# Performance work log

Hardware: AMD Instinct MI355X
Metric: run time of the kernel (lower is better)

The kernel has to match this reference:

```python
import jax, jax.numpy as jnp
import numpy as np
import math
from jax import lax

B, L = 64, 8192
S = L // 8          # width after 3 stride-(1,2) SAME convs
D = 4 * 5           # height(4) * channels(5) -> per-token feature dim
D_FLAT = S * D


def setup_inputs():
    key = jax.random.key(0)
    ks = jax.random.split(key, 32)
    sc = 0.1
    inp = {
        "inputs": jax.random.randint(ks[0], (B, L), 0, 4, dtype=jnp.int32),
        # conv stack: HWIO kernels, Conv2D(5,(4,4),(1,2),'SAME')
        "conv_w1": sc * jax.random.normal(ks[1], (4, 4, 1, 5), jnp.float32),
        "conv_b1": jnp.zeros((5,), jnp.float32),
        "conv_w2": sc * jax.random.normal(ks[2], (4, 4, 5, 5), jnp.float32),
        "conv_b2": jnp.zeros((5,), jnp.float32),
        "conv_w3": sc * jax.random.normal(ks[3], (4, 4, 5, 5), jnp.float32),
        "conv_b3": jnp.zeros((5,), jnp.float32),
        # 3 SelfAttn blocks, each with K/Q/V projections [D, D]
        "attn1_K": sc * jax.random.normal(ks[4], (D, D), jnp.float32),
        "attn1_Q": sc * jax.random.normal(ks[5], (D, D), jnp.float32),
        "attn1_V": sc * jax.random.normal(ks[6], (D, D), jnp.float32),
        "attn2_K": sc * jax.random.normal(ks[7], (D, D), jnp.float32),
        "attn2_Q": sc * jax.random.normal(ks[8], (D, D), jnp.float32),
        "attn2_V": sc * jax.random.normal(ks[9], (D, D), jnp.float32),
        "attn3_K": sc * jax.random.normal(ks[10], (D, D), jnp.float32),
        "attn3_Q": sc * jax.random.normal(ks[11], (D, D), jnp.float32),
        "attn3_V": sc * jax.random.normal(ks[12], (D, D), jnp.float32),
        # 3 Dense(10) layers (no activation, as in Keras defaults)
        "dense_w1": 0.01 * jax.random.normal(ks[13], (D_FLAT, 10), jnp.float32),
        "dense_b1": jnp.zeros((10,), jnp.float32),
        "dense_w2": sc * jax.random.normal(ks[14], (10, 10), jnp.float32),
        "dense_b2": jnp.zeros((10,), jnp.float32),
        "dense_w3": sc * jax.random.normal(ks[15], (10, 10), jnp.float32),
        "dense_b3": jnp.zeros((10,), jnp.float32),
    }
    return inp


def _conv(x, w, b):
    # NHWC, HWIO, strides (1,2), SAME
    y = lax.conv_general_dilated(x, w, window_strides=(1, 2), padding="SAME",
                                 dimension_numbers=("NHWC", "HWIO", "NHWC"))
    return y + b


def _self_attn(x, Kw, Qw, Vw):
    # x: [B, S, D]; manual causal scaled dot-product attention
    K = x @ Kw
    Q = x @ Qw
    V = x @ Vw
    s = Q.shape[1]
    mask = jnp.triu(jnp.full((s, s), -jnp.inf, dtype=x.dtype), k=1)
    scores = jnp.einsum("bsd,btd->bst", Q, K) / math.sqrt(K.shape[-1]) + mask
    return jax.nn.softmax(scores, axis=-1) @ V


def reference(inputs, conv_w1, conv_b1, conv_w2, conv_b2, conv_w3, conv_b3,
              attn1_K, attn1_Q, attn1_V, attn2_K, attn2_Q, attn2_V,
              attn3_K, attn3_Q, attn3_V,
              dense_w1, dense_b1, dense_w2, dense_b2, dense_w3, dense_b3):
    # one_hot over axis=1 -> [B, 4, L], then channel dim -> [B, 4, L, 1]
    x = jax.nn.one_hot(inputs, 4, axis=1, dtype=jnp.float32)[..., None]
    x = _conv(x, conv_w1, conv_b1)
    x = _conv(x, conv_w2, conv_b2)
    x = _conv(x, conv_w3, conv_b3)            # [B, 4, S, 5]
    # tokens along width, features = height(4) x channels(5)
    x = jnp.transpose(x, (0, 2, 1, 3)).reshape(x.shape[0], S, D)
    x = _self_attn(x, attn1_K, attn1_Q, attn1_V)
    x = _self_attn(x, attn2_K, attn2_Q, attn2_V)
    x = _self_attn(x, attn3_K, attn3_Q, attn3_V)
    x = x.reshape(x.shape[0], -1)             # flatten [B, S*D]
    x = x @ dense_w1 + dense_b1
    x = x @ dense_w2 + dense_b2
    x = x @ dense_w3 + dense_b3               # [B, 10]
    return x
```

## Files before the change

### kernel.cpp

```cpp
#include <hip/hip_runtime.h>
#include <hip/hip_bf16.h>


#define B_ 64
#define L_ 8192
#define S_ 1024
#define D_ 20

typedef unsigned short ushort_t;
typedef __attribute__((ext_vector_type(8))) short short8_t;
typedef __attribute__((ext_vector_type(4))) short short4_t;
typedef __attribute__((ext_vector_type(4))) float f32x4_t;

__device__ __forceinline__ ushort_t f2bf(float f) {
  unsigned u = __float_as_uint(f);
  return (ushort_t)((u + 0x7fffu + ((u >> 16) & 1u)) >> 16);
}
__device__ __forceinline__ float bf2f(ushort_t h) {
  return __uint_as_float(((unsigned)h) << 16);
}

__global__ __launch_bounds__(256) void conv12_kernel(
    const int* __restrict__ inp,
    const float* __restrict__ W1c, const float* __restrict__ B1c,
    const float* __restrict__ W2c, const float* __restrict__ B2c,
    float* __restrict__ out,
    const float* __restrict__ W1d,
    float* __restrict__ W1T,
    const float* __restrict__ B1d, const float* __restrict__ W2d,
    const float* __restrict__ B2d, const float* __restrict__ W3d,
    const float* __restrict__ B3d,
    float* __restrict__ outp) {
  __shared__ float w1s[80], b1s[5], w2s[400], b2s[5];
  for (int j = threadIdx.x; j < 400; j += 256) w2s[j] = W2c[j];
  if (threadIdx.x < 80)      w1s[threadIdx.x]      = W1c[threadIdx.x];
  else if (threadIdx.x < 85) b1s[threadIdx.x - 80] = B1c[threadIdx.x - 80];
  else if (threadIdx.x < 90) b2s[threadIdx.x - 85] = B2c[threadIdx.x - 85];
  __syncthreads();
  const int idx = blockIdx.x * 256 + threadIdx.x;
  const int b  = idx >> 11;
  const int wo = idx & 2047;
  const int* ib = inp + (size_t)b * L_;
  int iv[10];
#pragma unroll
  for (int t = 0; t < 10; ++t) {
    int g = 4 * wo - 3 + t;
    iv[t] = (g >= 0 && g < L_) ? ib[g] : -100;
  }
  float val[4][4][5];
#pragma unroll
  for (int pos = 0; pos < 4; ++pos) {
    const int w1 = 2 * wo - 1 + pos;
    const bool okp = (w1 >= 0 && w1 < 4096);
#pragma unroll
    for (int hi = 0; hi < 4; ++hi)
#pragma unroll
      for (int ci = 0; ci < 5; ++ci) val[hi][pos][ci] = okp ? b1s[ci] : 0.f;
    if (okp) {
#pragma unroll
      for (int kw = 0; kw < 4; ++kw) {
        const int gw = 2 * w1 - 1 + kw;
        if (gw >= 0 && gw < L_) {
          const int v = iv[2 * pos + kw];
#pragma unroll
          for (int hi = 0; hi < 4; ++hi) {
            const int kh = v - hi + 1;
            if (kh >= 0 && kh < 4) {
#pragma unroll
              for (int ci = 0; ci < 5; ++ci)
                val[hi][pos][ci] += w1s[(kh * 4 + kw) * 5 + ci];
            }
          }
        }
      }
    }
  }
  float acc[4][5];
#pragma unroll
  for (int h = 0; h < 4; ++h)
#pragma unroll
    for (int c = 0; c < 5; ++c) acc[h][c] = b2s[c];
#pragma unroll
  for (int kh = 0; kh < 4; ++kh)
#pragma unroll
    for (int kw = 0; kw < 4; ++kw)
#pragma unroll
      for (int ci = 0; ci < 5; ++ci) {
        const float* wp = w2s + ((kh * 4 + kw) * 5 + ci) * 5;
        float w0 = wp[0], w1v = wp[1], w2v = wp[2], w3 = wp[3], w4 = wp[4];
#pragma unroll
        for (int h = 0; h < 4; ++h) {
          int hi = h - 1 + kh;
          if (hi >= 0 && hi < 4) {
            float x = val[hi][kw][ci];
            acc[h][0] += w0 * x;  acc[h][1] += w1v * x; acc[h][2] += w2v * x;
            acc[h][3] += w3 * x;  acc[h][4] += w4 * x;
          }
        }
      }
  float* ob = out + (size_t)b * 4 * 2048 * 5;
#pragma unroll
  for (int h = 0; h < 4; ++h)
#pragma unroll
    for (int c = 0; c < 5; ++c) ob[(h * 2048 + wo) * 5 + c] = acc[h][c];
  for (int j = idx; j < 204800; j += 131072) {
    const int col = j / 20480, i2 = j - col * 20480;
    float w23[10];
#pragma unroll
    for (int k2 = 0; k2 < 10; ++k2) {
      float s = 0.f;
#pragma unroll
      for (int m = 0; m < 10; ++m) s += W2d[k2 * 10 + m] * W3d[m * 10 + col];
      w23[k2] = s;
    }
    float s = 0.f;
#pragma unroll
    for (int k2 = 0; k2 < 10; ++k2) s += W1d[i2 * 10 + k2] * w23[k2];
    W1T[j] = s;
  }
  if (idx < 640) {
    const int col = idx - (idx / 10) * 10;
    float bc = B3d[col];
#pragma unroll
    for (int m = 0; m < 10; ++m) bc += B2d[m] * W3d[m * 10 + col];
#pragma unroll
    for (int k2 = 0; k2 < 10; ++k2) {
      float w23 = 0.f;
#pragma unroll
      for (int m = 0; m < 10; ++m) w23 += W2d[k2 * 10 + m] * W3d[m * 10 + col];
      bc += B1d[k2] * w23;
    }
    outp[idx] = bc;
  }
}

__global__ __launch_bounds__(256) void conv3_proj_kernel(
    const float* __restrict__ in,
    const float* __restrict__ W,  const float* __restrict__ Bi,
    const float* __restrict__ Kw, const float* __restrict__ Qw,
    const float* __restrict__ Vw,
    ushort_t* __restrict__ Qb, ushort_t* __restrict__ Kb,
    ushort_t* __restrict__ Vt) {
  constexpr int WIN = 2048;
  __shared__ float ws[400], bs[5];
  __shared__ float kw[400], qw[400], vw[400];
  for (int j = threadIdx.x; j < 400; j += 256) {
    ws[j] = W[j]; kw[j] = Kw[j]; qw[j] = Qw[j]; vw[j] = Vw[j];
  }
  if (threadIdx.x < 5) bs[threadIdx.x] = Bi[threadIdx.x];
  __syncthreads();
  const int r  = blockIdx.x * 256 + threadIdx.x;
  const int b  = r >> 10;
  const int wo = r & 1023;
  float val[4][4][5];
#pragma unroll
  for (int hi = 0; hi < 4; ++hi) {
    const float* ir = in + ((size_t)b * 4 + hi) * WIN * 5;
#pragma unroll
    for (int kwp = 0; kwp < 4; ++kwp) {
      int wi = 2 * wo - 1 + kwp;
      bool ok = (wi >= 0 && wi < WIN);
#pragma unroll
      for (int ci = 0; ci < 5; ++ci) val[hi][kwp][ci] = ok ? ir[wi * 5 + ci] : 0.f;
    }
  }
  float acc[4][5];
#pragma unroll
  for (int h = 0; h < 4; ++h)
#pragma unroll
    for (int c = 0; c < 5; ++c) acc[h][c] = bs[c];
#pragma unroll
  for (int kh = 0; kh < 4; ++kh)
#pragma unroll
    for (int kwp = 0; kwp < 4; ++kwp)
#pragma unroll
      for (int ci = 0; ci < 5; ++ci) {
        const float* wp = ws + ((kh * 4 + kwp) * 5 + ci) * 5;
        float w0 = wp[0], w1 = wp[1], w2 = wp[2], w3 = wp[3], w4 = wp[4];
#pragma unroll
        for (int h = 0; h < 4; ++h) {
          int hi = h - 1 + kh;
          if (hi >= 0 && hi < 4) {
            float x = val[hi][kwp][ci];
            acc[h][0] += w0 * x; acc[h][1] += w1 * x; acc[h][2] += w2 * x;
            acc[h][3] += w3 * x; acc[h][4] += w4 * x;
          }
        }
      }
  float x[D_];
#pragma unroll
  for (int h = 0; h < 4; ++h)
#pragma unroll
    for (int c = 0; c < 5; ++c) x[h * 5 + c] = acc[h][c];
  float q[D_], k[D_], v[D_];
#pragma unroll
  for (int j = 0; j < D_; ++j) { q[j] = 0.f; k[j] = 0.f; v[j] = 0.f; }
#pragma unroll
  for (int i = 0; i < D_; ++i) {
#pragma unroll
    for (int j = 0; j < D_; ++j) {
      q[j] += x[i] * qw[i * D_ + j];
      k[j] += x[i] * kw[i * D_ + j];
      v[j] += x[i] * vw[i * D_ + j];
    }
  }
  const float sc = 0.22360679774997896f;
  ushort_t qt[32], kt[32];
#pragma unroll
  for (int j = 0; j < D_; ++j) { qt[j] = f2bf(q[j] * sc); kt[j] = f2bf(k[j]); }
#pragma unroll
  for (int j = D_; j < 32; ++j) { qt[j] = 0; kt[j] = 0; }
  int4* qd = (int4*)(Qb + (size_t)r * 32);
  int4* kd = (int4*)(Kb + (size_t)r * 32);
#pragma unroll
  for (int j = 0; j < 4; ++j) {
    qd[j] = *(const int4*)(qt + 8 * j);
    kd[j] = *(const int4*)(kt + 8 * j);
  }
  ushort_t* vbase = Vt + ((size_t)b * 32) * 1024 + wo;
#pragma unroll
  for (int d = 0; d < D_; ++d) vbase[d * 1024] = f2bf(v[d]);
}

template <bool FUSE>
__global__ __launch_bounds__(512, 6) void attn_kernel(
    const ushort_t* __restrict__ Qb, const ushort_t* __restrict__ Kb,
    const ushort_t* __restrict__ Vt,
    const float* __restrict__ Kw2, const float* __restrict__ Qw2,
    const float* __restrict__ Vw2,
    ushort_t* __restrict__ Qb2, ushort_t* __restrict__ Kb2,
    ushort_t* __restrict__ Vt2,
    const float* __restrict__ W1T,
    float* __restrict__ outp) {
  constexpr int VST = 1032;
  __shared__ ushort_t vts[20 * VST];
  __shared__ float extraf[FUSE ? 2480 : 1280];
  __shared__ float mrgL[64];
  __shared__ float red2[FUSE ? 4 : 40];
  const int blk   = blockIdx.x;
  const int b     = blk & 63;
  const int strip = 15 - (blk >> 6);
  const int q0    = strip * 64;
  const int nt    = q0 + 64;
  const int tid   = threadIdx.x;
  const int w     = tid >> 6;
  const int sub   = w & 3;
  const int half  = w >> 2;
  const int lane  = tid & 63;
  const int n     = lane & 15;
  const int quad  = lane >> 4;
  const int qbase = q0 + 16 * sub;
  const int qg    = qbase + n;
  const ushort_t* VtB = Vt + (size_t)b * 32 * 1024;
  const int ntc = nt >> 3;
  for (int i = tid; i < 20 * ntc; i += 512) {
    int row = i / ntc, cc = i - row * ntc;
    *(int4*)(vts + row * VST + cc * 8) =
        *(const int4*)(VtB + (size_t)row * 1024 + cc * 8);
  }
  if (FUSE) {
    for (int j = tid; j < 1200; j += 512) {
      int m = j / 400, oo = j - m * 400;
      extraf[j] = (m == 0) ? Kw2[oo] : (m == 1) ? Qw2[oo] : Vw2[oo];
    }
  }
  const ushort_t* KbB = Kb + (size_t)b * 1024 * 32;
  short8_t qfrag = *(const short8_t*)(Qb + ((size_t)(b * 1024 + qbase + n)) * 32 + quad * 8);
  f32x4_t oA = {0.f, 0.f, 0.f, 0.f};
  f32x4_t oB = {0.f, 0.f, 0.f, 0.f};
  const f32x4_t zero = {0.f, 0.f, 0.f, 0.f};
  float lsum = 0.f;
  const int nt2 = nt >> 1;
  const int tlo = half ? nt2 : 0;
  int thi = half ? nt : nt2;
  if (thi > qbase + 16) thi = qbase + 16;
  __syncthreads();
  for (int t0 = tlo; t0 < thi; t0 += 32) {
    short8_t kf0 = *(const short8_t*)(KbB + (size_t)(t0 + n) * 32 + quad * 8);
    short8_t kf1 = *(const short8_t*)(KbB + (size_t)(t0 + 16 + n) * 32 + quad * 8);
#pragma unroll
    for (int c = 0; c < 2; ++c) {
      const int tg = t0 + c * 16 + quad * 4;
      f32x4_t s = __builtin_amdgcn_mfma_f32_16x16x32_bf16(c ? kf1 : kf0, qfrag,
                                                          zero, 0, 0, 0);
      ushort_t pk4[4];
#pragma unroll
      for (int r = 0; r < 4; ++r) {
        float p = (tg + r <= qg) ? __expf(s[r]) : 0.f;
        ushort_t h = f2bf(p);
        lsum += bf2f(h);
        pk4[r] = h;
      }
      short4_t pfrag = *(const short4_t*)pk4;
      short4_t vlo = *(const short4_t*)(vts + n * VST + t0 + c * 16 + quad * 4);
      short4_t vhi = *(const short4_t*)(vts + (16 + (n & 3)) * VST + t0 + c * 16 + quad * 4);
      oA = __builtin_amdgcn_mfma_f32_16x16x16bf16_1k(vlo, pfrag, oA, 0, 0, 0);
      oB = __builtin_amdgcn_mfma_f32_16x16x16bf16_1k(vhi, pfrag, oB, 0, 0, 0);
    }
  }
  float l = lsum;
  l += __shfl_xor(l, 16, 64);
  l += __shfl_xor(l, 32, 64);
  float* ox  = FUSE ? (extraf + 1200) : extraf;
  float* oxw = ox + sub * 320;
  if (half) {
#pragma unroll
    for (int r = 0; r < 4; ++r) oxw[n * 20 + quad * 4 + r] = oA[r];
    if (quad == 0) {
#pragma unroll
      for (int r = 0; r < 4; ++r) oxw[n * 20 + 16 + r] = oB[r];
      mrgL[sub * 16 + n] = l;
    }
  }
  __syncthreads();
  if (!half) {
#pragma unroll
    for (int r = 0; r < 4; ++r) oA[r] += oxw[n * 20 + quad * 4 + r];
    if (quad == 0) {
#pragma unroll
      for (int r = 0; r < 4; ++r) oB[r] += oxw[n * 20 + 16 + r];
    }
    l += mrgL[sub * 16 + n];
    const float inv = 1.f / l;
#pragma unroll
    for (int r = 0; r < 4; ++r) oxw[n * 20 + quad * 4 + r] = oA[r] * inv;
    if (quad == 0) {
#pragma unroll
      for (int r = 0; r < 4; ++r) oxw[n * 20 + 16 + r] = oB[r] * inv;
    }
  }
  if (FUSE) {
    if (!half) {
      float* pw = extraf;
      __asm__ volatile("s_waitcnt lgkmcnt(0)" ::: "memory");
      const int row  = lane >> 2;
      const int part = lane & 3;
      float x[D_];
#pragma unroll
      for (int i = 0; i < D_; ++i) x[i] = oxw[row * 20 + i];
      float qv[5], kv[5], vv[5];
#pragma unroll
      for (int jj = 0; jj < 5; ++jj) { qv[jj] = 0.f; kv[jj] = 0.f; vv[jj] = 0.f; }
#pragma unroll
      for (int i = 0; i < D_; ++i) {
        const float xi = x[i];
#pragma unroll
        for (int jj = 0; jj < 5; ++jj) {
          const int j = 5 * part + jj;
          kv[jj] += xi * pw[i * 20 + j];
          qv[jj] += xi * pw[400 + i * 20 + j];
          vv[jj] += xi * pw[800 + i * 20 + j];
        }
      }
      const float sc = 0.22360679774997896f;
      const int rg = b * 1024 + qbase + row;
      const int s  = rg & 1023;
#pragma unroll
      for (int jj = 0; jj < 5; ++jj) {
        const int j = 5 * part + jj;
        Kb2[(size_t)rg * 32 + j] = f2bf(kv[jj]);
        Qb2[(size_t)rg * 32 + j] = f2bf(qv[jj] * sc);
        Vt2[(size_t)b * 32768 + (size_t)j * 1024 + s] = f2bf(vv[jj]);
      }
      if (part == 0) {
#pragma unroll
        for (int u = 0; u < 6; ++u)
          *(unsigned*)(Kb2 + (size_t)rg * 32 + 20 + 2 * u) = 0u;
      } else if (part == 1) {
#pragma unroll
        for (int u = 0; u < 6; ++u)
          *(unsigned*)(Qb2 + (size_t)rg * 32 + 20 + 2 * u) = 0u;
      }
    }
  } else {
    __syncthreads();
    float acc[10];
#pragma unroll
    for (int j = 0; j < 10; ++j) acc[j] = 0.f;
    const int base = q0 * 20;
    if (tid < 256) {
#pragma unroll
      for (int k = 0; k < 5; ++k) {
        const int il = tid + 256 * k;
        const float xv = ox[il];
#pragma unroll
        for (int j = 0; j < 10; ++j)
          acc[j] += xv * W1T[(size_t)j * 20480 + base + il];
      }
    }
#pragma unroll
    for (int off = 1; off < 64; off <<= 1) {
#pragma unroll
      for (int j = 0; j < 10; ++j) acc[j] += __shfl_xor(acc[j], off, 64);
    }
    if (tid < 256 && lane == 0) {
#pragma unroll
      for (int j = 0; j < 10; ++j) red2[w * 10 + j] = acc[j];
    }
    __syncthreads();
    if (tid < 10) {
      float s2 = red2[tid] + red2[10 + tid] + red2[20 + tid] + red2[30 + tid];
      atomicAdd(&outp[b * 10 + tid], s2);
    }
  }
}

extern "C" void kernel_launch(void* const* d_in, const int* in_sizes, int n_in,
                              void* d_out, int out_size, void* d_ws, size_t ws_size,
                              hipStream_t stream) {
  const int*   inp = (const int*)d_in[0];
  const float* cw1 = (const float*)d_in[1];
  const float* cb1 = (const float*)d_in[2];
  const float* cw2 = (const float*)d_in[3];
  const float* cb2 = (const float*)d_in[4];
  const float* cw3 = (const float*)d_in[5];
  const float* cb3 = (const float*)d_in[6];
  const float* a1K = (const float*)d_in[7];
  const float* a1Q = (const float*)d_in[8];
  const float* a1V = (const float*)d_in[9];
  const float* a2K = (const float*)d_in[10];
  const float* a2Q = (const float*)d_in[11];
  const float* a2V = (const float*)d_in[12];
  const float* a3K = (const float*)d_in[13];
  const float* a3Q = (const float*)d_in[14];
  const float* a3V = (const float*)d_in[15];
  const float* dw1 = (const float*)d_in[16];
  const float* db1 = (const float*)d_in[17];
  const float* dw2 = (const float*)d_in[18];
  const float* db2 = (const float*)d_in[19];
  const float* dw3 = (const float*)d_in[20];
  const float* db3 = (const float*)d_in[21];
  float* outp = (float*)d_out;

  float* wsf = (float*)d_ws;
  ushort_t* qbA  = (ushort_t*)(wsf);
  ushort_t* kbA  = (ushort_t*)(wsf + 1048576);
  ushort_t* vtA  = (ushort_t*)(wsf + 2097152);
  float*    w1t  = wsf + 4466688;
  ushort_t* qbB  = (ushort_t*)(wsf + 4671488);
  ushort_t* kbB  = (ushort_t*)(wsf + 5712384);
  ushort_t* vtB  = (ushort_t*)(wsf + 6760960);
  float*    c2   = wsf + 5242880;

  conv12_kernel<<<512, 256, 0, stream>>>(inp, cw1, cb1, cw2, cb2, c2, dw1,
                                         w1t, db1, dw2, db2, dw3, db3, outp);

  conv3_proj_kernel<<<256, 256, 0, stream>>>(c2, cw3, cb3, a1K, a1Q, a1V,
                                             qbA, kbA, vtA);
  attn_kernel<true><<<1024, 512, 0, stream>>>(
      qbA, kbA, vtA, a2K, a2Q, a2V, qbB, kbB, vtB, nullptr, nullptr);
  attn_kernel<true><<<1024, 512, 0, stream>>>(
      qbB, kbB, vtB, a3K, a3Q, a3V, qbA, kbA, vtA, nullptr, nullptr);
  attn_kernel<false><<<1024, 512, 0, stream>>>(
      qbA, kbA, vtA, nullptr, nullptr, nullptr, nullptr, nullptr, nullptr,
      w1t, outp);
}
```

Measured before the change: 196.9 us.

## Fuse conv1-2 and conv3+QKV projection into one kernel via shared-memory tile

Merges the conv1/conv2 kernel and the conv3+projection kernel into a single launch. Each 512-thread block computes 514 conv2 output columns (a 256-wide tile plus halo) into shared memory, then half the threads run conv3 and the Q/K/V projection from that tile. This removes one kernel launch and the global round-trip of the conv2 intermediate, at the cost of recomputing two halo columns per tile, leaving half the threads idle in the second phase, and using fewer blocks.

```diff
diff --git a/kernel.cpp b/kernel.cpp
--- a/kernel.cpp
+++ b/kernel.cpp
@@ -20,11 +20,15 @@
   return __uint_as_float(((unsigned)h) << 16);
 }
 
-__global__ __launch_bounds__(256) void conv12_kernel(
+__global__ __launch_bounds__(512) void conv_fused_kernel(
     const int* __restrict__ inp,
     const float* __restrict__ W1c, const float* __restrict__ B1c,
     const float* __restrict__ W2c, const float* __restrict__ B2c,
-    float* __restrict__ out,
+    const float* __restrict__ W3c, const float* __restrict__ B3c,
+    const float* __restrict__ Kw,  const float* __restrict__ Qw,
+    const float* __restrict__ Vw,
+    ushort_t* __restrict__ Qb, ushort_t* __restrict__ Kb,
+    ushort_t* __restrict__ Vt,
     const float* __restrict__ W1d,
     float* __restrict__ W1T,
     const float* __restrict__ B1d, const float* __restrict__ W2d,
@@ -32,78 +36,168 @@
     const float* __restrict__ B3d,
     float* __restrict__ outp) {
   __shared__ float w1s[80], b1s[5], w2s[400], b2s[5];
-  for (int j = threadIdx.x; j < 400; j += 256) w2s[j] = W2c[j];
-  if (threadIdx.x < 80)      w1s[threadIdx.x]      = W1c[threadIdx.x];
-  else if (threadIdx.x < 85) b1s[threadIdx.x - 80] = B1c[threadIdx.x - 80];
-  else if (threadIdx.x < 90) b2s[threadIdx.x - 85] = B2c[threadIdx.x - 85];
+  __shared__ float ws3[400], bs3[5];
+  __shared__ float kws[400], qws[400], vws[400];
+  __shared__ float c2s[514 * 21];
+  const int tid = threadIdx.x;
+  const int blk = blockIdx.x;
+  for (int i = tid; i < 400; i += 512) {
+    w2s[i] = W2c[i]; ws3[i] = W3c[i];
+    kws[i] = Kw[i];  qws[i] = Qw[i];  vws[i] = Vw[i];
+  }
+  if (tid < 80)       w1s[tid]      = W1c[tid];
+  else if (tid < 85)  b1s[tid - 80] = B1c[tid - 80];
+  else if (tid < 90)  b2s[tid - 85] = B2c[tid - 85];
+  else if (tid < 95)  bs3[tid - 90] = B3c[tid - 90];
   __syncthreads();
-  const int idx = blockIdx.x * 256 + threadIdx.x;
-  const int b  = idx >> 11;
-  const int wo = idx & 2047;
+  const int b   = blk >> 2;
+  const int wo0 = (blk & 3) << 8;
   const int* ib = inp + (size_t)b * L_;
-  int iv[10];
-#pragma unroll
-  for (int t = 0; t < 10; ++t) {
-    int g = 4 * wo - 3 + t;
-    iv[t] = (g >= 0 && g < L_) ? ib[g] : -100;
-  }
-  float val[4][4][5];
-#pragma unroll
-  for (int pos = 0; pos < 4; ++pos) {
-    const int w1 = 2 * wo - 1 + pos;
-    const bool okp = (w1 >= 0 && w1 < 4096);
-#pragma unroll
-    for (int hi = 0; hi < 4; ++hi)
-#pragma unroll
-      for (int ci = 0; ci < 5; ++ci) val[hi][pos][ci] = okp ? b1s[ci] : 0.f;
-    if (okp) {
-#pragma unroll
-      for (int kw = 0; kw < 4; ++kw) {
-        const int gw = 2 * w1 - 1 + kw;
-        if (gw >= 0 && gw < L_) {
-          const int v = iv[2 * pos + kw];
-#pragma unroll
-          for (int hi = 0; hi < 4; ++hi) {
-            const int kh = v - hi + 1;
-            if (kh >= 0 && kh < 4) {
-#pragma unroll
-              for (int ci = 0; ci < 5; ++ci)
-                val[hi][pos][ci] += w1s[(kh * 4 + kw) * 5 + ci];
+#pragma unroll 1
+  for (int sidx = tid; sidx < 514; sidx += 512) {
+    const int wi = 2 * wo0 - 1 + sidx;
+    float acc[4][5];
+    if (wi >= 0 && wi < 2048) {
+      int iv[10];
+#pragma unroll
+      for (int t = 0; t < 10; ++t) {
+        int g = 4 * wi - 3 + t;
+        iv[t] = (g >= 0 && g < L_) ? ib[g] : -100;
+      }
+      float val[4][4][5];
+#pragma unroll
+      for (int pos = 0; pos < 4; ++pos) {
+        const int w1 = 2 * wi - 1 + pos;
+        const bool okp = (w1 >= 0 && w1 < 4096);
+#pragma unroll
+        for (int hi = 0; hi < 4; ++hi)
+#pragma unroll
+          for (int ci = 0; ci < 5; ++ci) val[hi][pos][ci] = okp ? b1s[ci] : 0.f;
+        if (okp) {
+#pragma unroll
+          for (int kw = 0; kw < 4; ++kw) {
+            const int gw = 2 * w1 - 1 + kw;
+            if (gw >= 0 && gw < L_) {
+              const int v = iv[2 * pos + kw];
+#pragma unroll
+              for (int hi = 0; hi < 4; ++hi) {
+                const int kh = v - hi + 1;
+                if (kh >= 0 && kh < 4) {
+#pragma unroll
+                  for (int ci = 0; ci < 5; ++ci)
+                    val[hi][pos][ci] += w1s[(kh * 4 + kw) * 5 + ci];
+                }
+              }
             }
           }
         }
       }
-    }
-  }
-  float acc[4][5];
-#pragma unroll
-  for (int h = 0; h < 4; ++h)
-#pragma unroll
-    for (int c = 0; c < 5; ++c) acc[h][c] = b2s[c];
-#pragma unroll
-  for (int kh = 0; kh < 4; ++kh)
-#pragma unroll
-    for (int kw = 0; kw < 4; ++kw)
-#pragma unroll
-      for (int ci = 0; ci < 5; ++ci) {
-        const float* wp = w2s + ((kh * 4 + kw) * 5 + ci) * 5;
-        float w0 = wp[0], w1v = wp[1], w2v = wp[2], w3 = wp[3], w4 = wp[4];
-#pragma unroll
-        for (int h = 0; h < 4; ++h) {
-          int hi = h - 1 + kh;
-          if (hi >= 0 && hi < 4) {
-            float x = val[hi][kw][ci];
-            acc[h][0] += w0 * x;  acc[h][1] += w1v * x; acc[h][2] += w2v * x;
-            acc[h][3] += w3 * x;  acc[h][4] += w4 * x;
+#pragma unroll
+      for (int h = 0; h < 4; ++h)
+#pragma unroll
+        for (int c = 0; c < 5; ++c) acc[h][c] = b2s[c];
+#pragma unroll
+      for (int kh = 0; kh < 4; ++kh)
+#pragma unroll
+        for (int kw = 0; kw < 4; ++kw)
+#pragma unroll
+          for (int ci = 0; ci < 5; ++ci) {
+            const float* wp = w2s + ((kh * 4 + kw) * 5 + ci) * 5;
+            float w0 = wp[0], w1v = wp[1], w2v = wp[2], w3v = wp[3], w4v = wp[4];
+#pragma unroll
+            for (int h = 0; h < 4; ++h) {
+              int hi = h - 1 + kh;
+              if (hi >= 0 && hi < 4) {
+                float x = val[hi][kw][ci];
+                acc[h][0] += w0 * x;  acc[h][1] += w1v * x; acc[h][2] += w2v * x;
+                acc[h][3] += w3v * x; acc[h][4] += w4v * x;
+              }
+            }
+          }
+    } else {
+#pragma unroll
+      for (int h = 0; h < 4; ++h)
+#pragma unroll
+        for (int c = 0; c < 5; ++c) acc[h][c] = 0.f;
+    }
+#pragma unroll
+    for (int h = 0; h < 4; ++h)
+#pragma unroll
+      for (int c = 0; c < 5; ++c) c2s[sidx * 21 + h * 5 + c] = acc[h][c];
+  }
+  __syncthreads();
+  if (tid < 256) {
+    const int wo = wo0 + tid;
+    const int r  = (b << 10) + wo;
+    float val[4][4][5];
+#pragma unroll
+    for (int kwp = 0; kwp < 4; ++kwp) {
+      const int lidx = 2 * tid + kwp;
+#pragma unroll
+      for (int hi = 0; hi < 4; ++hi)
+#pragma unroll
+        for (int ci = 0; ci < 5; ++ci)
+          val[hi][kwp][ci] = c2s[lidx * 21 + hi * 5 + ci];
+    }
+    float acc[4][5];
+#pragma unroll
+    for (int h = 0; h < 4; ++h)
+#pragma unroll
+      for (int c = 0; c < 5; ++c) acc[h][c] = bs3[c];
+#pragma unroll
+    for (int kh = 0; kh < 4; ++kh)
+#pragma unroll
+      for (int kwp = 0; kwp < 4; ++kwp)
+#pragma unroll
+        for (int ci = 0; ci < 5; ++ci) {
+          const float* wp = ws3 + ((kh * 4 + kwp) * 5 + ci) * 5;
+          float w0 = wp[0], w1 = wp[1], w2 = wp[2], w3 = wp[3], w4 = wp[4];
+#pragma unroll
+          for (int h = 0; h < 4; ++h) {
+            int hi = h - 1 + kh;
+            if (hi >= 0 && hi < 4) {
+              float x = val[hi][kwp][ci];
+              acc[h][0] += w0 * x; acc[h][1] += w1 * x; acc[h][2] += w2 * x;
+              acc[h][3] += w3 * x; acc[h][4] += w4 * x;
+            }
           }
         }
-      }
-  float* ob = out + (size_t)b * 4 * 2048 * 5;
-#pragma unroll
-  for (int h = 0; h < 4; ++h)
-#pragma unroll
-    for (int c = 0; c < 5; ++c) ob[(h * 2048 + wo) * 5 + c] = acc[h][c];
-  for (int j = idx; j < 204800; j += 131072) {
+    float x[D_];
+#pragma unroll
+    for (int h = 0; h < 4; ++h)
+#pragma unroll
+      for (int c = 0; c < 5; ++c) x[h * 5 + c] = acc[h][c];
+    float q[D_], k[D_], v[D_];
+#pragma unroll
+    for (int j = 0; j < D_; ++j) { q[j] = 0.f; k[j] = 0.f; v[j] = 0.f; }
+#pragma unroll
+    for (int i = 0; i < D_; ++i) {
+#pragma unroll
+      for (int j = 0; j < D_; ++j) {
+        q[j] += x[i] * qws[i * D_ + j];
+        k[j] += x[i] * kws[i * D_ + j];
+        v[j] += x[i] * vws[i * D_ + j];
+      }
+    }
+    const float sc = 0.22360679774997896f;
+    ushort_t qt[32], kt[32];
+#pragma unroll
+    for (int j = 0; j < D_; ++j) { qt[j] = f2bf(q[j] * sc); kt[j] = f2bf(k[j]); }
+#pragma unroll
+    for (int j = D_; j < 32; ++j) { qt[j] = 0; kt[j] = 0; }
+    int4* qd = (int4*)(Qb + (size_t)r * 32);
+    int4* kd = (int4*)(Kb + (size_t)r * 32);
+#pragma unroll
+    for (int j = 0; j < 4; ++j) {
+      qd[j] = *(const int4*)(qt + 8 * j);
+      kd[j] = *(const int4*)(kt + 8 * j);
+    }
+    ushort_t* vbase = Vt + ((size_t)b * 32) * 1024 + wo;
+#pragma unroll
+    for (int d = 0; d < D_; ++d) vbase[d * 1024] = f2bf(v[d]);
+  }
+  const int gidx = blk * 512 + tid;
+  for (int j = gidx; j < 204800; j += 131072) {
     const int col = j / 20480, i2 = j - col * 20480;
     float w23[10];
 #pragma unroll
@@ -118,8 +212,8 @@
     for (int k2 = 0; k2 < 10; ++k2) s += W1d[i2 * 10 + k2] * w23[k2];
     W1T[j] = s;
   }
-  if (idx < 640) {
-    const int col = idx - (idx / 10) * 10;
+  if (gidx < 640) {
+    const int col = gidx - (gidx / 10) * 10;
     float bc = B3d[col];
 #pragma unroll
     for (int m = 0; m < 10; ++m) bc += B2d[m] * W3d[m * 10 + col];
@@ -130,96 +224,8 @@
       for (int m = 0; m < 10; ++m) w23 += W2d[k2 * 10 + m] * W3d[m * 10 + col];
       bc += B1d[k2] * w23;
     }
-    outp[idx] = bc;
-  }
-}
-
-__global__ __launch_bounds__(256) void conv3_proj_kernel(
-    const float* __restrict__ in,
-    const float* __restrict__ W,  const float* __restrict__ Bi,
-    const float* __restrict__ Kw, const float* __restrict__ Qw,
-    const float* __restrict__ Vw,
-    ushort_t* __restrict__ Qb, ushort_t* __restrict__ Kb,
-    ushort_t* __restrict__ Vt) {
-  constexpr int WIN = 2048;
-  __shared__ float ws[400], bs[5];
-  __shared__ float kw[400], qw[400], vw[400];
-  for (int j = threadIdx.x; j < 400; j += 256) {
-    ws[j] = W[j]; kw[j] = Kw[j]; qw[j] = Qw[j]; vw[j] = Vw[j];
-  }
-  if (threadIdx.x < 5) bs[threadIdx.x] = Bi[threadIdx.x];
-  __syncthreads();
-  const int r  = blockIdx.x * 256 + threadIdx.x;
-  const int b  = r >> 10;
-  const int wo = r & 1023;
-  float val[4][4][5];
-#pragma unroll
-  for (int hi = 0; hi < 4; ++hi) {
-    const float* ir = in + ((size_t)b * 4 + hi) * WIN * 5;
-#pragma unroll
-    for (int kwp = 0; kwp < 4; ++kwp) {
-      int wi = 2 * wo - 1 + kwp;
-      bool ok = (wi >= 0 && wi < WIN);
-#pragma unroll
-      for (int ci = 0; ci < 5; ++ci) val[hi][kwp][ci] = ok ? ir[wi * 5 + ci] : 0.f;
-    }
-  }
-  float acc[4][5];
-#pragma unroll
-  for (int h = 0; h < 4; ++h)
-#pragma unroll
-    for (int c = 0; c < 5; ++c) acc[h][c] = bs[c];
-#pragma unroll
-  for (int kh = 0; kh < 4; ++kh)
-#pragma unroll
-    for (int kwp = 0; kwp < 4; ++kwp)
-#pragma unroll
-      for (int ci = 0; ci < 5; ++ci) {
-        const float* wp = ws + ((kh * 4 + kwp) * 5 + ci) * 5;
-        float w0 = wp[0], w1 = wp[1], w2 = wp[2], w3 = wp[3], w4 = wp[4];
-#pragma unroll
-        for (int h = 0; h < 4; ++h) {
-          int hi = h - 1 + kh;
-          if (hi >= 0 && hi < 4) {
-            float x = val[hi][kwp][ci];
-            acc[h][0] += w0 * x; acc[h][1] += w1 * x; acc[h][2] += w2 * x;
-            acc[h][3] += w3 * x; acc[h][4] += w4 * x;
-          }
-        }
-      }
-  float x[D_];
-#pragma unroll
-  for (int h = 0; h < 4; ++h)
-#pragma unroll
-    for (int c = 0; c < 5; ++c) x[h * 5 + c] = acc[h][c];
-  float q[D_], k[D_], v[D_];
-#pragma unroll
-  for (int j = 0; j < D_; ++j) { q[j] = 0.f; k[j] = 0.f; v[j] = 0.f; }
-#pragma unroll
-  for (int i = 0; i < D_; ++i) {
-#pragma unroll
-    for (int j = 0; j < D_; ++j) {
-      q[j] += x[i] * qw[i * D_ + j];
-      k[j] += x[i] * kw[i * D_ + j];
-      v[j] += x[i] * vw[i * D_ + j];
-    }
-  }
-  const float sc = 0.22360679774997896f;
-  ushort_t qt[32], kt[32];
-#pragma unroll
-  for (int j = 0; j < D_; ++j) { qt[j] = f2bf(q[j] * sc); kt[j] = f2bf(k[j]); }
-#pragma unroll
-  for (int j = D_; j < 32; ++j) { qt[j] = 0; kt[j] = 0; }
-  int4* qd = (int4*)(Qb + (size_t)r * 32);
-  int4* kd = (int4*)(Kb + (size_t)r * 32);
-#pragma unroll
-  for (int j = 0; j < 4; ++j) {
-    qd[j] = *(const int4*)(qt + 8 * j);
-    kd[j] = *(const int4*)(kt + 8 * j);
-  }
-  ushort_t* vbase = Vt + ((size_t)b * 32) * 1024 + wo;
-#pragma unroll
-  for (int d = 0; d < D_; ++d) vbase[d * 1024] = f2bf(v[d]);
+    outp[gidx] = bc;
+  }
 }
 
 template <bool FUSE>
@@ -440,13 +446,10 @@
   ushort_t* qbB  = (ushort_t*)(wsf + 4671488);
   ushort_t* kbB  = (ushort_t*)(wsf + 5712384);
   ushort_t* vtB  = (ushort_t*)(wsf + 6760960);
-  float*    c2   = wsf + 5242880;
-
-  conv12_kernel<<<512, 256, 0, stream>>>(inp, cw1, cb1, cw2, cb2, c2, dw1,
-                                         w1t, db1, dw2, db2, dw3, db3, outp);
-
-  conv3_proj_kernel<<<256, 256, 0, stream>>>(c2, cw3, cb3, a1K, a1Q, a1V,
-                                             qbA, kbA, vtA);
+
+  conv_fused_kernel<<<256, 512, 0, stream>>>(
+      inp, cw1, cb1, cw2, cb2, cw3, cb3, a1K, a1Q, a1V, qbA, kbA, vtA,
+      dw1, w1t, db1, dw2, db2, dw3, db3, outp);
   attn_kernel<true><<<1024, 512, 0, stream>>>(
       qbA, kbA, vtA, a2K, a2Q, a2V, qbB, kbB, vtB, nullptr, nullptr);
   attn_kernel<true><<<1024, 512, 0, stream>>>(
```

New measurement: 495.3 us. 2.52x slower.
